# Optimization experiments

Hardware: AMD Instinct MI355X
Metric: run time of the kernel (lower is better)

The kernel has to match this reference:

```python
import jax, jax.numpy as jnp
import numpy as np

B, L, H, NUM_LABELS = 4, 256, 768, 13


def setup_inputs() -> dict:
    key = jax.random.key(0)
    k1, k2, k3, k4, k5 = jax.random.split(key, 5)
    s1 = 1.0 / np.sqrt(2 * H)
    s2 = 1.0 / np.sqrt(H)
    return {
        "hidden_states": jax.random.normal(k1, (B, L, H), dtype=jnp.float32),
        "W1": jax.random.uniform(k2, (2 * H, H), jnp.float32, -s1, s1),
        "b1": jax.random.uniform(k3, (H,), jnp.float32, -s1, s1),
        "W2": jax.random.uniform(k4, (H, NUM_LABELS), jnp.float32, -s2, s2),
        "b2": jax.random.uniform(k5, (NUM_LABELS,), jnp.float32, -s2, s2),
    }


def reference(hidden_states, W1, b1, W2, b2):
    # Original: ffn(cat([x_start expand over dim2, x_end expand over dim1], -1))
    # Algebraically: Linear(2H->H) on the concat == proj(x_start) + proj(x_end)
    # broadcast over the L x L span grid, avoiding the (B,L,L,2H) tensor.
    H_ = hidden_states.shape[-1]
    xs_proj = jnp.einsum('bsh,hk->bsk', hidden_states, W1[:H_])   # start half
    xe_proj = jnp.einsum('bsh,hk->bsk', hidden_states, W1[H_:])   # end half
    h = xs_proj[:, :, None, :] + xe_proj[:, None, :, :] + b1      # (B,L,L,H)
    h = jax.nn.gelu(h, approximate=False)                         # torch GELU default = exact erf
    logits = jnp.einsum('bijk,kn->bijn', h, W2) + b2              # (B,L,L,num_labels)
    return logits
```

## Files before the change

### kernel.cpp

```cpp
#include <hip/hip_runtime.h>
#include <math.h>

#define H 768
#define L 256
#define NB 4
#define NL 13

typedef _Float16 h2 __attribute__((ext_vector_type(2)));
typedef _Float16 half8 __attribute__((ext_vector_type(8)));
typedef float f32x4 __attribute__((ext_vector_type(4)));

__device__ inline h2 gelu_pk(h2 x) {
    const _Float16 kC = (_Float16)3.75f;
    h2 hi = {kC, kC}, lo = {(_Float16)-3.75f, (_Float16)-3.75f};
    h2 xc = __builtin_elementwise_min(__builtin_elementwise_max(x, lo), hi);
    h2 u = xc * xc;
    const _Float16 kE = (_Float16)0.125f;
    h2 ve = {kE, kE};
    h2 v = u * ve;
    const _Float16 d4v = (_Float16)0.0832840f,  d3v = (_Float16)-0.4335206f;
    const _Float16 d2v = (_Float16)0.8960128f,  d1v = (_Float16)-0.9876456f;
    const _Float16 d0v = (_Float16)0.7946463f;
    h2 d4 = {d4v, d4v}, d3 = {d3v, d3v}, d2 = {d2v, d2v}, d1 = {d1v, d1v}, d0 = {d0v, d0v};
    h2 p = v * (v * (v * (v * d4 + d3) + d2) + d1) + d0;
    h2 t = xc * p;
    const _Float16 kH = (_Float16)0.5f;
    h2 halfv = {kH, kH};
    h2 hx = x * halfv;
    return hx * t + hx;
}

__global__ __launch_bounds__(256) void prep_kernel(
    const float* __restrict__ X, const float* __restrict__ W1,
    const float* __restrict__ W2,
    _Float16* __restrict__ Afrag, _Float16* __restrict__ Bfrag1,
    _Float16* __restrict__ Bfrag2)
{
    const int blk = blockIdx.x;
    const int tid = threadIdx.x;

    if (blk < 384) {
        int t = blk * 256 + tid;
        int lane = t & 63;
        int g = t >> 6;
        int kb = g % 24, mt = g / 24;
        int m = mt * 16 + (lane & 15);
        int k0 = kb * 32 + (lane >> 4) * 8;
        const float* px = X + (size_t)m * H + k0;
        float4 a = *(const float4*)px;
        float4 b = *(const float4*)(px + 4);
        half8 o = { (_Float16)a.x, (_Float16)a.y, (_Float16)a.z, (_Float16)a.w,
                    (_Float16)b.x, (_Float16)b.y, (_Float16)b.z, (_Float16)b.w };
        *(half8*)(Afrag + (size_t)t * 8) = o;
    } else if (blk < 960) {
        int t = (blk - 384) * 256 + tid;
        int lane = t & 63;
        int g = t >> 6;
        int kb = g % 24, ntg = g / 24;
        int np = ntg * 16 + (lane & 15);
        int k0 = kb * 32 + (lane >> 4) * 8;
        const float* Wb = W1 + ((np >= H) ? (size_t)H * H : 0);
        int c = np - ((np >= H) ? H : 0);
        half8 o;
        #pragma unroll
        for (int u = 0; u < 8; ++u)
            o[u] = (_Float16)Wb[(size_t)(k0 + u) * H + c];
        *(half8*)(Bfrag1 + (size_t)t * 8) = o;
    } else {
        int base = (blk - 960) * 768 + tid;
        #pragma unroll
        for (int r = 0; r < 3; ++r) {
            int idx = base + r * 256;
            int u = idx & 7;
            int lane = (idx >> 3) & 63;
            int kb = idx >> 9;
            int k = kb * 32 + ((lane >> 4) << 3) + u;
            int n = lane & 15;
            float v = (n < NL) ? W2[(size_t)k * NL + n] : 0.f;
            Bfrag2[idx] = (_Float16)v;
        }
    }
}

__global__ __launch_bounds__(256) void gemm_mfma(
    const _Float16* __restrict__ Afrag, const _Float16* __restrict__ Bfrag1,
    const float* __restrict__ b1, _Float16* __restrict__ Pxs2,
    _Float16* __restrict__ Pxe)
{
    const int tid = threadIdx.x;
    const int w = tid >> 6, lane = tid & 63;
    const int ln = lane & 15, quad = lane >> 4;
    const int m0 = blockIdx.x * 64 + (w & 1) * 32;
    const int n0g = blockIdx.y * 64 + (w >> 1) * 32;
    const int mt0 = m0 >> 4, ntg0 = n0g >> 4;

    const half8* pa0 = (const half8*)(Afrag + (((size_t)mt0 * 24) * 64 + lane) * 8);
    const half8* pa1 = (const half8*)(Afrag + ((((size_t)mt0 + 1) * 24) * 64 + lane) * 8);
    const half8* pb0 = (const half8*)(Bfrag1 + (((size_t)ntg0 * 24) * 64 + lane) * 8);
    const half8* pb1 = (const half8*)(Bfrag1 + ((((size_t)ntg0 + 1) * 24) * 64 + lane) * 8);

    f32x4 acc[2][2] = {};
    #pragma unroll 4
    for (int kb = 0; kb < 24; ++kb) {
        half8 a0 = pa0[kb * 64];
        half8 a1 = pa1[kb * 64];
        half8 b0 = pb0[kb * 64];
        half8 b1v = pb1[kb * 64];
        acc[0][0] = __builtin_amdgcn_mfma_f32_16x16x32_f16(a0, b0, acc[0][0], 0, 0, 0);
        acc[0][1] = __builtin_amdgcn_mfma_f32_16x16x32_f16(a0, b1v, acc[0][1], 0, 0, 0);
        acc[1][0] = __builtin_amdgcn_mfma_f32_16x16x32_f16(a1, b0, acc[1][0], 0, 0, 0);
        acc[1][1] = __builtin_amdgcn_mfma_f32_16x16x32_f16(a1, b1v, acc[1][1], 0, 0, 0);
    }

    if (n0g < H) {
        float bv[2] = { b1[n0g + ln], b1[n0g + 16 + ln] };
        #pragma unroll
        for (int mt = 0; mt < 2; ++mt)
            #pragma unroll
            for (int nt = 0; nt < 2; ++nt) {
                int n = n0g + nt * 16 + ln;
                #pragma unroll
                for (int r = 0; r < 4; ++r) {
                    int m = m0 + mt * 16 + quad * 4 + r;
                    Pxs2[(size_t)m * H + n] = (_Float16)(acc[mt][nt][r] + bv[nt]);
                }
            }
    } else {
        #pragma unroll
        for (int mt = 0; mt < 2; ++mt)
            #pragma unroll
            for (int nt = 0; nt < 2; ++nt) {
                int n = n0g - H + nt * 16 + ln;
                #pragma unroll
                for (int r = 0; r < 4; ++r) {
                    int m = m0 + mt * 16 + quad * 4 + r;
                    Pxe[(size_t)m * H + n] = (_Float16)acc[mt][nt][r];
                }
            }
    }
}

__global__ __launch_bounds__(256, 4) void span_mfma_kernel(
    const _Float16* __restrict__ Pxs2, const _Float16* __restrict__ Pxe,
    const _Float16* __restrict__ Bfrag2, const float* __restrict__ b2,
    float* __restrict__ out)
{
    __shared__ unsigned int xsf[4 * H / 2];
    const int ip = blockIdx.x >> 2;
    const int jq = blockIdx.x & 3;
    const int bi0 = ip * 4;
    const int b = bi0 >> 8;
    const int tid = threadIdx.x;

    const unsigned int* xsrc = (const unsigned int*)(Pxs2 + (size_t)bi0 * H);
    #pragma unroll
    for (int t = 0; t < 6; ++t) xsf[t * 256 + tid] = xsrc[t * 256 + tid];

    const int wave = tid >> 6;
    const int lane = tid & 63;
    const int n = lane & 15;
    const int quad = lane >> 4;
    const int j_load = jq * 64 + wave * 16 + n;

    const _Float16* xerow = Pxe + (size_t)(b * L + j_load) * H + quad * 8;
    const half8* bptr = (const half8*)(Bfrag2 + (size_t)lane * 8);

    f32x4 acc[4] = {};
    __syncthreads();

    for (int kb = 0; kb < H / 32; ++kb) {
        half8 bfrag = bptr[kb * 64];
        uint4 xev = *(const uint4*)(xerow + kb * 32);
        h2 xep[4] = { __builtin_bit_cast(h2, xev.x), __builtin_bit_cast(h2, xev.y),
                      __builtin_bit_cast(h2, xev.z), __builtin_bit_cast(h2, xev.w) };
        const int xo = kb * 16 + quad * 4;

        #pragma unroll
        for (int i01 = 0; i01 < 4; ++i01) {
            uint4 xsd = *(const uint4*)&xsf[i01 * (H / 2) + xo];
            h2 xsp[4] = { __builtin_bit_cast(h2, xsd.x), __builtin_bit_cast(h2, xsd.y),
                          __builtin_bit_cast(h2, xsd.z), __builtin_bit_cast(h2, xsd.w) };
            unsigned int pk[4];
            #pragma unroll
            for (int p = 0; p < 4; ++p) {
                h2 g = gelu_pk(xsp[p] + xep[p]);
                pk[p] = __builtin_bit_cast(unsigned int, g);
            }
            uint4 pk4 = {pk[0], pk[1], pk[2], pk[3]};
            half8 afrag = __builtin_bit_cast(half8, pk4);
            acc[i01] = __builtin_amdgcn_mfma_f32_16x16x32_f16(afrag, bfrag, acc[i01], 0, 0, 0);
        }
    }

    if (n < NL) {
        float b2v = b2[n];
        #pragma unroll
        for (int i01 = 0; i01 < 4; ++i01)
            #pragma unroll
            for (int r = 0; r < 4; ++r) {
                int j = jq * 64 + wave * 16 + quad * 4 + r;
                out[((size_t)(bi0 + i01) * L + j) * NL + n] = acc[i01][r] + b2v;
            }
    }
}

extern "C" void kernel_launch(void* const* d_in, const int* in_sizes, int n_in,
                              void* d_out, int out_size, void* d_ws, size_t ws_size,
                              hipStream_t stream)
{
    (void)in_sizes; (void)n_in; (void)out_size; (void)ws_size;
    const float* X  = (const float*)d_in[0];
    const float* W1 = (const float*)d_in[1];
    const float* b1 = (const float*)d_in[2];
    const float* W2 = (const float*)d_in[3];
    const float* b2 = (const float*)d_in[4];
    float* out = (float*)d_out;

    char* ws = (char*)d_ws;
    _Float16* Pxs2   = (_Float16*)ws;
    _Float16* Pxe    = Pxs2 + (size_t)NB * L * H;
    _Float16* Afrag  = Pxe + (size_t)NB * L * H;
    _Float16* Bfrag1 = Afrag + (size_t)NB * L * H;
    _Float16* Bfrag2 = Bfrag1 + (size_t)2 * H * H;

    prep_kernel<<<976, 256, 0, stream>>>(X, W1, W2, Afrag, Bfrag1, Bfrag2);
    gemm_mfma<<<dim3(16, 24), 256, 0, stream>>>(Afrag, Bfrag1, b1, Pxs2, Pxe);
    span_mfma_kernel<<<NB * L, 256, 0, stream>>>(Pxs2, Pxe, Bfrag2, b2, out);
}
```

Measured before the change: 123.7 us.

## Fuse fp16 conversion into GEMM via LDS tiles, dropping separate prep kernel

Replaces the prep kernel that wrote pre-swizzled fp16 fragments of X and W1 to global memory with a GEMM that loads fp32 tiles directly, converts to fp16 and stages them in shared-memory tiles. The W2 fragment packing moves into an extra grid row of the same launch. This removes a kernel launch and a global-memory round trip of the converted operands. In exchange it adds LDS staging, two barriers per k-step, and transposed 2-byte LDS stores for W1 that may bank-conflict.

```diff
diff --git a/kernel.cpp b/kernel.cpp
--- a/kernel.cpp
+++ b/kernel.cpp
@@ -7,6 +7,7 @@
 #define NL 13
 
 typedef _Float16 h2 __attribute__((ext_vector_type(2)));
+typedef _Float16 h4 __attribute__((ext_vector_type(4)));
 typedef _Float16 half8 __attribute__((ext_vector_type(8)));
 typedef float f32x4 __attribute__((ext_vector_type(4)));
 
@@ -30,44 +31,16 @@
     return hx * t + hx;
 }
 
-__global__ __launch_bounds__(256) void prep_kernel(
+__global__ __launch_bounds__(256) void gemm_fused(
     const float* __restrict__ X, const float* __restrict__ W1,
-    const float* __restrict__ W2,
-    _Float16* __restrict__ Afrag, _Float16* __restrict__ Bfrag1,
+    const float* __restrict__ b1, const float* __restrict__ W2,
+    _Float16* __restrict__ Pxs2, _Float16* __restrict__ Pxe,
     _Float16* __restrict__ Bfrag2)
 {
-    const int blk = blockIdx.x;
     const int tid = threadIdx.x;
 
-    if (blk < 384) {
-        int t = blk * 256 + tid;
-        int lane = t & 63;
-        int g = t >> 6;
-        int kb = g % 24, mt = g / 24;
-        int m = mt * 16 + (lane & 15);
-        int k0 = kb * 32 + (lane >> 4) * 8;
-        const float* px = X + (size_t)m * H + k0;
-        float4 a = *(const float4*)px;
-        float4 b = *(const float4*)(px + 4);
-        half8 o = { (_Float16)a.x, (_Float16)a.y, (_Float16)a.z, (_Float16)a.w,
-                    (_Float16)b.x, (_Float16)b.y, (_Float16)b.z, (_Float16)b.w };
-        *(half8*)(Afrag + (size_t)t * 8) = o;
-    } else if (blk < 960) {
-        int t = (blk - 384) * 256 + tid;
-        int lane = t & 63;
-        int g = t >> 6;
-        int kb = g % 24, ntg = g / 24;
-        int np = ntg * 16 + (lane & 15);
-        int k0 = kb * 32 + (lane >> 4) * 8;
-        const float* Wb = W1 + ((np >= H) ? (size_t)H * H : 0);
-        int c = np - ((np >= H) ? H : 0);
-        half8 o;
-        #pragma unroll
-        for (int u = 0; u < 8; ++u)
-            o[u] = (_Float16)Wb[(size_t)(k0 + u) * H + c];
-        *(half8*)(Bfrag1 + (size_t)t * 8) = o;
-    } else {
-        int base = (blk - 960) * 768 + tid;
+    if (blockIdx.y == 24) {
+        int base = blockIdx.x * 768 + tid;
         #pragma unroll
         for (int r = 0; r < 3; ++r) {
             int idx = base + r * 256;
@@ -79,49 +52,76 @@
             float v = (n < NL) ? W2[(size_t)k * NL + n] : 0.f;
             Bfrag2[idx] = (_Float16)v;
         }
-    }
-}
-
-__global__ __launch_bounds__(256) void gemm_mfma(
-    const _Float16* __restrict__ Afrag, const _Float16* __restrict__ Bfrag1,
-    const float* __restrict__ b1, _Float16* __restrict__ Pxs2,
-    _Float16* __restrict__ Pxe)
-{
-    const int tid = threadIdx.x;
+        return;
+    }
+
+    __shared__ _Float16 As[64][72];
+    __shared__ _Float16 Bs[64][72];
     const int w = tid >> 6, lane = tid & 63;
     const int ln = lane & 15, quad = lane >> 4;
-    const int m0 = blockIdx.x * 64 + (w & 1) * 32;
-    const int n0g = blockIdx.y * 64 + (w >> 1) * 32;
-    const int mt0 = m0 >> 4, ntg0 = n0g >> 4;
-
-    const half8* pa0 = (const half8*)(Afrag + (((size_t)mt0 * 24) * 64 + lane) * 8);
-    const half8* pa1 = (const half8*)(Afrag + ((((size_t)mt0 + 1) * 24) * 64 + lane) * 8);
-    const half8* pb0 = (const half8*)(Bfrag1 + (((size_t)ntg0 * 24) * 64 + lane) * 8);
-    const half8* pb1 = (const half8*)(Bfrag1 + ((((size_t)ntg0 + 1) * 24) * 64 + lane) * 8);
+    const int m0 = blockIdx.x * 64;
+    const int n0g = blockIdx.y * 64;
+    const bool isE = (n0g >= H);
+    const float* Wb = W1 + (isE ? (size_t)H * H : 0);
+    const int c0 = isE ? (n0g - H) : n0g;
+
+    const int ar = tid >> 4;
+    const int ac = (tid & 15) * 4;
+    const int bc = (tid & 15) * 4;
 
     f32x4 acc[2][2] = {};
-    #pragma unroll 4
-    for (int kb = 0; kb < 24; ++kb) {
-        half8 a0 = pa0[kb * 64];
-        half8 a1 = pa1[kb * 64];
-        half8 b0 = pb0[kb * 64];
-        half8 b1v = pb1[kb * 64];
-        acc[0][0] = __builtin_amdgcn_mfma_f32_16x16x32_f16(a0, b0, acc[0][0], 0, 0, 0);
-        acc[0][1] = __builtin_amdgcn_mfma_f32_16x16x32_f16(a0, b1v, acc[0][1], 0, 0, 0);
-        acc[1][0] = __builtin_amdgcn_mfma_f32_16x16x32_f16(a1, b0, acc[1][0], 0, 0, 0);
-        acc[1][1] = __builtin_amdgcn_mfma_f32_16x16x32_f16(a1, b1v, acc[1][1], 0, 0, 0);
-    }
-
-    if (n0g < H) {
-        float bv[2] = { b1[n0g + ln], b1[n0g + 16 + ln] };
+    for (int kr = 0; kr < H / 64; ++kr) {
+        const int k0 = kr * 64;
+        #pragma unroll
+        for (int r = 0; r < 4; ++r) {
+            int arow = r * 16 + ar;
+            float4 f = *(const float4*)&X[(size_t)(m0 + arow) * H + k0 + ac];
+            h4 o = { (_Float16)f.x, (_Float16)f.y, (_Float16)f.z, (_Float16)f.w };
+            *(h4*)&As[arow][ac] = o;
+        }
+        #pragma unroll
+        for (int r = 0; r < 2; ++r) {
+            int kpl = r * 16 + (tid >> 4);
+            const float* wr = &Wb[(size_t)(k0 + 2 * kpl) * H + c0 + bc];
+            float4 fa = *(const float4*)wr;
+            float4 fb = *(const float4*)(wr + H);
+            h2 p0 = {(_Float16)fa.x, (_Float16)fb.x};
+            h2 p1 = {(_Float16)fa.y, (_Float16)fb.y};
+            h2 p2 = {(_Float16)fa.z, (_Float16)fb.z};
+            h2 p3 = {(_Float16)fa.w, (_Float16)fb.w};
+            *(h2*)&Bs[bc + 0][2 * kpl] = p0;
+            *(h2*)&Bs[bc + 1][2 * kpl] = p1;
+            *(h2*)&Bs[bc + 2][2 * kpl] = p2;
+            *(h2*)&Bs[bc + 3][2 * kpl] = p3;
+        }
+        __syncthreads();
+        #pragma unroll
+        for (int sub = 0; sub < 2; ++sub) {
+            const int ko = sub * 32 + quad * 8;
+            half8 a0 = *(const half8*)&As[(w & 1) * 32 + ln][ko];
+            half8 a1 = *(const half8*)&As[(w & 1) * 32 + 16 + ln][ko];
+            half8 b0 = *(const half8*)&Bs[(w >> 1) * 32 + ln][ko];
+            half8 b1f = *(const half8*)&Bs[(w >> 1) * 32 + 16 + ln][ko];
+            acc[0][0] = __builtin_amdgcn_mfma_f32_16x16x32_f16(a0, b0, acc[0][0], 0, 0, 0);
+            acc[0][1] = __builtin_amdgcn_mfma_f32_16x16x32_f16(a0, b1f, acc[0][1], 0, 0, 0);
+            acc[1][0] = __builtin_amdgcn_mfma_f32_16x16x32_f16(a1, b0, acc[1][0], 0, 0, 0);
+            acc[1][1] = __builtin_amdgcn_mfma_f32_16x16x32_f16(a1, b1f, acc[1][1], 0, 0, 0);
+        }
+        __syncthreads();
+    }
+
+    const int mb = m0 + (w & 1) * 32;
+    const int nb = (w >> 1) * 32;
+    if (!isE) {
+        float bv[2] = { b1[n0g + nb + ln], b1[n0g + nb + 16 + ln] };
         #pragma unroll
         for (int mt = 0; mt < 2; ++mt)
             #pragma unroll
             for (int nt = 0; nt < 2; ++nt) {
-                int n = n0g + nt * 16 + ln;
+                int n = n0g + nb + nt * 16 + ln;
                 #pragma unroll
                 for (int r = 0; r < 4; ++r) {
-                    int m = m0 + mt * 16 + quad * 4 + r;
+                    int m = mb + mt * 16 + quad * 4 + r;
                     Pxs2[(size_t)m * H + n] = (_Float16)(acc[mt][nt][r] + bv[nt]);
                 }
             }
@@ -130,10 +130,10 @@
         for (int mt = 0; mt < 2; ++mt)
             #pragma unroll
             for (int nt = 0; nt < 2; ++nt) {
-                int n = n0g - H + nt * 16 + ln;
+                int n = c0 + nb + nt * 16 + ln;
                 #pragma unroll
                 for (int r = 0; r < 4; ++r) {
-                    int m = m0 + mt * 16 + quad * 4 + r;
+                    int m = mb + mt * 16 + quad * 4 + r;
                     Pxe[(size_t)m * H + n] = (_Float16)acc[mt][nt][r];
                 }
             }
@@ -219,11 +219,8 @@
     char* ws = (char*)d_ws;
     _Float16* Pxs2   = (_Float16*)ws;
     _Float16* Pxe    = Pxs2 + (size_t)NB * L * H;
-    _Float16* Afrag  = Pxe + (size_t)NB * L * H;
-    _Float16* Bfrag1 = Afrag + (size_t)NB * L * H;
-    _Float16* Bfrag2 = Bfrag1 + (size_t)2 * H * H;
-
-    prep_kernel<<<976, 256, 0, stream>>>(X, W1, W2, Afrag, Bfrag1, Bfrag2);
-    gemm_mfma<<<dim3(16, 24), 256, 0, stream>>>(Afrag, Bfrag1, b1, Pxs2, Pxe);
+    _Float16* Bfrag2 = Pxe + (size_t)NB * L * H;
+
+    gemm_fused<<<dim3(16, 25), 256, 0, stream>>>(X, W1, b1, W2, Pxs2, Pxe, Bfrag2);
     span_mfma_kernel<<<NB * L, 256, 0, stream>>>(Pxs2, Pxe, Bfrag2, b2, out);
 }
```

Measured after the change: 123.8 us. No clear change (+0.1%).
